# Performance work log

Measured on AMD Instinct MI355X. Metric: run time of the kernel, lower is better.

The kernel has to match this reference:

```python
import jax, jax.numpy as jnp
import numpy as np

B, T, DIM, UNITS, OUT = 64, 240, 512, 1024, 75


def setup_inputs() -> dict:
    key = jax.random.key(0)
    keys = iter(jax.random.split(key, 40))

    def w(shape, scale=0.05):
        return jax.random.normal(next(keys), shape, dtype=jnp.float32) * scale

    inp = {
        "in_audio": w((B, T, DIM), 1.0),   # per-step CNN audio features
        "curr_step": w((B, OUT), 1.0),      # initial motion pose
    }

    def add_cell(name, in_dim, u):
        inp[name + "_Wx"] = w((in_dim, 4 * u))
        inp[name + "_Wh"] = w((u, 4 * u))
        inp[name + "_b"] = jnp.zeros((4 * u,), jnp.float32)

    add_cell("enc1", DIM, UNITS)
    add_cell("enc2", UNITS, UNITS)
    add_cell("enc3", UNITS, UNITS)
    inp["fc_W"] = w((UNITS, DIM))
    inp["fc_b"] = jnp.zeros((DIM,), jnp.float32)
    add_cell("dec1", OUT + DIM, UNITS)
    add_cell("dec2", UNITS, UNITS)
    add_cell("dec3", UNITS, UNITS)
    inp["out_W"] = w((UNITS, OUT))
    inp["out_b"] = jnp.zeros((OUT,), jnp.float32)
    return inp


def _lstm(x, h, c, Wx, Wh, b):
    # standard LSTM cell, gate order i, f, g, o
    z = x @ Wx + h @ Wh + b                      # [B, 4U]
    i, f, g, o = jnp.split(z, 4, axis=-1)
    c_new = jax.nn.sigmoid(f) * c + jax.nn.sigmoid(i) * jnp.tanh(g)
    h_new = jax.nn.sigmoid(o) * jnp.tanh(c_new)
    return h_new, c_new


def reference(in_audio, curr_step,
              enc1_Wx, enc1_Wh, enc1_b,
              enc2_Wx, enc2_Wh, enc2_b,
              enc3_Wx, enc3_Wh, enc3_b,
              fc_W, fc_b,
              dec1_Wx, dec1_Wh, dec1_b,
              dec2_Wx, dec2_Wh, dec2_b,
              dec3_Wx, dec3_Wh, dec3_b,
              out_W, out_b):
    Bn = in_audio.shape[0]
    dt = in_audio.dtype
    zu = jnp.zeros((Bn, UNITS), dt)
    carry = (curr_step,
             zu, zu, zu, zu, zu, zu,   # eh1,ec1,eh2,ec2,eh3,ec3
             zu, zu, zu, zu, zu, zu)   # dh1,dc1,dh2,dc2,dh3,dc3

    def step(carry, x):
        (curr, eh1, ec1, eh2, ec2, eh3, ec3,
         dh1, dc1, dh2, dc2, dh3, dc3) = carry
        eh1, ec1 = _lstm(x, eh1, ec1, enc1_Wx, enc1_Wh, enc1_b)
        eh2, ec2 = _lstm(eh1, eh2, ec2, enc2_Wx, enc2_Wh, enc2_b)
        eh3, ec3 = _lstm(eh2, eh3, ec3, enc3_Wx, enc3_Wh, enc3_b)
        _h = jnp.tanh(eh3 @ fc_W + fc_b)          # bottleneck audio code [B, DIM]
        d_in = jnp.concatenate([curr, _h], axis=-1)  # [B, OUT+DIM]
        dh1, dc1 = _lstm(d_in, dh1, dc1, dec1_Wx, dec1_Wh, dec1_b)
        dh2, dc2 = _lstm(dh1, dh2, dc2, dec2_Wx, dec2_Wh, dec2_b)
        dh3, dc3 = _lstm(dh2, dh3, dc3, dec3_Wx, dec3_Wh, dec3_b)
        y = jax.nn.elu(dh3 @ out_W + out_b)       # next motion step [B, OUT]
        new_carry = (y, eh1, ec1, eh2, ec2, eh3, ec3,
                     dh1, dc1, dh2, dc2, dh3, dc3)
        return new_carry, y

    _, ys = jax.lax.scan(step, carry, jnp.swapaxes(in_audio, 0, 1))
    return jnp.swapaxes(ys, 0, 1)  # [B, T, OUT]
```

## Files before the change

kernel.cpp:

```cpp
#include <hip/hip_runtime.h>
#include <hip/hip_bf16.h>
#include <hip/hip_cooperative_groups.h>

namespace cg = cooperative_groups;

typedef __bf16 bf16;
typedef __bf16 bf16x8 __attribute__((ext_vector_type(8)));
typedef float  floatx4 __attribute__((ext_vector_type(4)));
typedef unsigned int uint32;

#define NB   64
#define NT   240
#define NDIM 512
#define NU   1024
#define NOUT 75
#define NWG  64
#define NTHR 1024

#define HSLOT (64 * 1024)
#define YW    80
#define YSLOT (64 * YW)
#define BW    528
#define BSLOT (64 * BW)

struct Params {
  const float* curr;
  const float* bias[8];
  const bf16*  pk[8];
  const bf16*  audio_bf;
  bf16* hr[6];
  bf16* ybuf;
  bf16* hbot;
  uint32* arrv;
  uint32* gof;
  float* out;
  int rmask;
  int pmask;
};

__device__ __forceinline__ float sigmoidf_(float x) { return 1.f / (1.f + __expf(-x)); }

__device__ __forceinline__ void gbar(uint32* arrv, uint32 sc, int w, int tid)
{
  asm volatile("s_waitcnt vmcnt(0)" ::: "memory");
  __syncthreads();
  if (tid == 0)
    __hip_atomic_store(&arrv[w * 32], sc, __ATOMIC_RELAXED, __HIP_MEMORY_SCOPE_AGENT);
  if (tid < NWG) {
    int spin = 0;
    while (__hip_atomic_load(&arrv[tid * 32], __ATOMIC_RELAXED, __HIP_MEMORY_SCOPE_AGENT) < sc) {
      __builtin_amdgcn_s_sleep(1);
      if (++spin > (1 << 24)) break;
    }
  }
  __syncthreads();
}

template<int ST0, int B1, int ST1, int B2, int ST2, int KTOT, int KREAL>
__device__ void lstm_cell(const bf16* __restrict__ p0, const bf16* __restrict__ p1,
                          const bf16* __restrict__ p2,
                          const bf16* __restrict__ pack, const float* __restrict__ bias,
                          bf16* __restrict__ hout, float& ccr,
                          float (* __restrict__ zbuf)[64][16], bf16 (* __restrict__ hstage)[16],
                          char* __restrict__ cb0, char* __restrict__ cb1,
                          char* __restrict__ cb2, char* __restrict__ cb3,
                          int w, int tid)
{
  const int lane = tid & 63, wid = tid >> 6;
  const int g = wid & 3, v = wid >> 2;
  const int lq = lane >> 4, lr = lane & 15;
  constexpr int NCH = KTOT / 128;

  auto issue = [&](int J, char* bufp) {
    #pragma unroll
    for (int ii = 0; ii < 2; ++ii) {
      const int idx = 2 * wid + ii;
      const int kb  = (idx >> 2) & 3;
      const int sel = idx & 3;
      if (idx < 16) {
        int kq = J * 128 + kb * 32 + lq * 8;
        if constexpr (KREAL < KTOT) { if (kq >= KREAL) kq = B2; }
        const int row = 16 * sel + lr;
        const bf16* src;
        if (kq < B1)      src = p0 + (size_t)row * ST0 + kq;
        else if (kq < B2) src = p1 + (size_t)row * ST1 + (kq - B1);
        else              src = p2 + (size_t)row * ST2 + (kq - B2);
        __builtin_amdgcn_global_load_lds((const uint32*)src,
            (uint32*)(bufp + (kb * 4 + sel) * 1024), 16, 0, 0);
      } else {
        const int kq8 = J * 16 + kb * 4 + lq;
        const bf16* src = pack + ((size_t)kq8 * 4096 + 1024 * sel + 16 * w + lr) * 8;
        __builtin_amdgcn_global_load_lds((const uint32*)src,
            (uint32*)(bufp + 16384 + (kb * 4 + sel) * 1024), 16, 0, 0);
      }
    }
  };

  floatx4 c = {0.f, 0.f, 0.f, 0.f};
  auto compute = [&](const char* bufp) {
    #pragma unroll
    for (int kb = 0; kb < 4; ++kb) {
      bf16x8 af  = *(const bf16x8*)(bufp + (kb * 4 + v) * 1024 + lane * 16);
      bf16x8 bfr = *(const bf16x8*)(bufp + 16384 + (kb * 4 + g) * 1024 + lane * 16);
      c = __builtin_amdgcn_mfma_f32_16x16x32_bf16(af, bfr, c, 0, 0, 0);
    }
  };

  char *pA = cb0, *pB = cb1, *pC = cb2, *pD = cb3;
  issue(0, pA);
  issue(1, pB);
  issue(2, pC);
  for (int J = 0; J + 3 < NCH; ++J) {
    asm volatile("s_waitcnt vmcnt(4)" ::: "memory");
    __builtin_amdgcn_s_barrier();
    asm volatile("" ::: "memory");
    issue(J + 3, pD);
    compute(pA);
    char* t = pA; pA = pB; pB = pC; pC = pD; pD = t;
  }
  asm volatile("s_waitcnt vmcnt(4)" ::: "memory");
  __builtin_amdgcn_s_barrier();
  asm volatile("" ::: "memory");
  compute(pA);
  { char* t = pA; pA = pB; pB = pC; pC = pD; pD = t; }
  asm volatile("s_waitcnt vmcnt(2)" ::: "memory");
  __builtin_amdgcn_s_barrier();
  asm volatile("" ::: "memory");
  compute(pA);
  { char* t = pA; pA = pB; pB = pC; pC = pD; pD = t; }
  asm volatile("s_waitcnt vmcnt(0)" ::: "memory");
  __builtin_amdgcn_s_barrier();
  asm volatile("" ::: "memory");
  compute(pA);

  #pragma unroll
  for (int r = 0; r < 4; ++r)
    zbuf[g][16 * v + lq * 4 + r][lr] = c[r];
  __syncthreads();
  {
    const int m = tid >> 4, u = tid & 15;
    const int uc = 16 * w + u;
    const float zi = zbuf[0][m][u] + bias[uc];
    const float zf = zbuf[1][m][u] + bias[NU + uc];
    const float zg = zbuf[2][m][u] + bias[2 * NU + uc];
    const float zo = zbuf[3][m][u] + bias[3 * NU + uc];
    const float cold = ccr;
    const float cn = sigmoidf_(zf) * cold + sigmoidf_(zi) * tanhf(zg);
    ccr = cn;
    hstage[m][u] = (bf16)(sigmoidf_(zo) * tanhf(cn));
  }
  __syncthreads();
  if (tid < 512) {
    const int m = tid >> 3, up = tid & 7;
    const uint32 vv = *(const uint32*)&hstage[m][2 * up];
    __hip_atomic_store((uint32*)(hout + (size_t)m * NU + 16 * w) + up, vv,
                       __ATOMIC_RELAXED, __HIP_MEMORY_SCOPE_AGENT);
  }
}

template<int NEFF>
__device__ void gemm_small(const bf16* __restrict__ a, const bf16* __restrict__ pack,
                           float (* __restrict__ zbuf)[64][16], int w, int tid)
{
  const int lane = tid & 63, wid = tid >> 6;
  const int v = wid & 3, s = wid >> 2;
  const int lr = lane & 15, lq = lane >> 4;
  const int n0 = 16 * w;

  const bf16* wbase = pack + ((size_t)lq * NEFF + (n0 + lr)) * 8;

  bf16x8 wreg[8];
  #pragma unroll
  for (int i = 0; i < 8; ++i)
    wreg[i] = *(const bf16x8*)(wbase + (size_t)(s + 4 * i) * (4 * NEFF * 8));

  floatx4 c = {0.f,0.f,0.f,0.f};
  const bf16* ab = a + (size_t)(16 * v + lr) * NU;

  bf16x8 xa[2];
  xa[0] = *(const bf16x8*)(ab + s * 32 + lq * 8);
  #pragma unroll
  for (int i = 0; i < 8; ++i) {
    const int cur = i & 1, nxt = cur ^ 1;
    if (i + 1 < 8)
      xa[nxt] = *(const bf16x8*)(ab + (s + 4 * (i + 1)) * 32 + lq * 8);
    c = __builtin_amdgcn_mfma_f32_16x16x32_bf16(xa[cur], wreg[i], c, 0, 0, 0);
  }

  #pragma unroll
  for (int r = 0; r < 4; ++r) zbuf[s][16 * v + lq * 4 + r][lr] = c[r];
  __syncthreads();
}

extern "C" __global__ void __launch_bounds__(NTHR)
dancer_main(Params p)
{
  __shared__ __align__(16) char cbuf[4][32768];
  __shared__ float zbuf[4][64][16];
  __shared__ bf16  hstage[64][16];
  cg::grid_group grid = cg::this_grid();
  const int tid = threadIdx.x;
  const int w = blockIdx.x;
  const int gtid = w * NTHR + tid;
  const int rmask = p.rmask, pmask = p.pmask;

  float cc0 = 0.f, cc1 = 0.f, cc2 = 0.f, cc3 = 0.f, cc4 = 0.f, cc5 = 0.f;

  if (tid == 0) {
    p.arrv[w * 32] = 0;
    if (w == 0) *p.gof = 0;
  }
  for (int i = gtid; i < 6 * NB * NU; i += NWG * NTHR) {
    const int b = i >> 16, off = i & 65535;
    p.hr[b][(size_t)rmask * HSLOT + off] = (bf16)0.f;
  }
  for (int i = gtid; i < NB * YW; i += NWG * NTHR) {
    const int m = i / YW, c = i - m * YW;
    p.ybuf[i] = (c < NOUT) ? (bf16)p.curr[m * NOUT + c] : (bf16)0.f;
  }
  for (int i = gtid; i < (rmask + 1) * NB * 16; i += NWG * NTHR) {
    const int slot = i >> 10, m = (i >> 4) & 63, cix = i & 15;
    p.hbot[(size_t)slot * BSLOT + (size_t)m * BW + 512 + cix] = (bf16)0.f;
  }
  __syncthreads();
  grid.sync();

  uint32 sc = 1;
  for (int t = 0; t < NT; ++t) {
    const int st_ = t & rmask;
    const int sp_ = (t - 1) & rmask;
    __syncthreads();

    lstm_cell<NT * NDIM, NDIM, NU, NDIM, NU, NDIM + NU, NDIM + NU>(
        p.audio_bf + t * NDIM, p.hr[0] + (size_t)sp_ * HSLOT, p.hr[0] + (size_t)sp_ * HSLOT,
        p.pk[0], p.bias[0], p.hr[0] + (size_t)st_ * HSLOT, cc0, zbuf, &hstage[0],
        cbuf[0], cbuf[1], cbuf[2], cbuf[3], w, tid);
    gbar(p.arrv, sc++, w, tid);

    lstm_cell<NU, NU, NU, NU, NU, 2 * NU, 2 * NU>(
        p.hr[0] + (size_t)st_ * HSLOT, p.hr[1] + (size_t)sp_ * HSLOT, p.hr[1] + (size_t)sp_ * HSLOT,
        p.pk[1], p.bias[1], p.hr[1] + (size_t)st_ * HSLOT, cc1, zbuf, &hstage[0],
        cbuf[0], cbuf[1], cbuf[2], cbuf[3], w, tid);
    gbar(p.arrv, sc++, w, tid);

    lstm_cell<NU, NU, NU, NU, NU, 2 * NU, 2 * NU>(
        p.hr[1] + (size_t)st_ * HSLOT, p.hr[2] + (size_t)sp_ * HSLOT, p.hr[2] + (size_t)sp_ * HSLOT,
        p.pk[2], p.bias[2], p.hr[2] + (size_t)st_ * HSLOT, cc2, zbuf, &hstage[0],
        cbuf[0], cbuf[1], cbuf[2], cbuf[3], w, tid);
    gbar(p.arrv, sc++, w, tid);

    if (w < 32) {
      gemm_small<512>(p.hr[2] + (size_t)st_ * HSLOT, p.pk[3], zbuf, w, tid);
      const int m = tid >> 4, u = tid & 15;
      const float z = zbuf[0][m][u] + zbuf[1][m][u] + zbuf[2][m][u] + zbuf[3][m][u]
                      + p.bias[3][16 * w + u];
      hstage[m][u] = (bf16)tanhf(z);
      __syncthreads();
      if (tid < 512) {
        const int m2 = tid >> 3, up = tid & 7;
        const uint32 v = *(const uint32*)&hstage[m2][2 * up];
        __hip_atomic_store((uint32*)(p.hbot + (size_t)st_ * BSLOT + (size_t)m2 * BW + 16 * w) + up,
                           v, __ATOMIC_RELAXED, __HIP_MEMORY_SCOPE_AGENT);
      }
    }
    gbar(p.arrv, sc++, w, tid);

    lstm_cell<YW, YW, BW, YW + BW, NU, 1664, YW + BW + NU>(
        p.ybuf + (size_t)st_ * YSLOT, p.hbot + (size_t)st_ * BSLOT, p.hr[3] + (size_t)sp_ * HSLOT,
        p.pk[4], p.bias[4], p.hr[3] + (size_t)st_ * HSLOT, cc3, zbuf, &hstage[0],
        cbuf[0], cbuf[1], cbuf[2], cbuf[3], w, tid);
    gbar(p.arrv, sc++, w, tid);

    lstm_cell<NU, NU, NU, NU, NU, 2 * NU, 2 * NU>(
        p.hr[3] + (size_t)st_ * HSLOT, p.hr[4] + (size_t)sp_ * HSLOT, p.hr[4] + (size_t)sp_ * HSLOT,
        p.pk[5], p.bias[5], p.hr[4] + (size_t)st_ * HSLOT, cc4, zbuf, &hstage[0],
        cbuf[0], cbuf[1], cbuf[2], cbuf[3], w, tid);
    gbar(p.arrv, sc++, w, tid);

    lstm_cell<NU, NU, NU, NU, NU, 2 * NU, 2 * NU>(
        p.hr[4] + (size_t)st_ * HSLOT, p.hr[5] + (size_t)sp_ * HSLOT, p.hr[5] + (size_t)sp_ * HSLOT,
        p.pk[6], p.bias[6], p.hr[5] + (size_t)st_ * HSLOT, cc5, zbuf, &hstage[0],
        cbuf[0], cbuf[1], cbuf[2], cbuf[3], w, tid);
    gbar(p.arrv, sc++, w, tid);

    if (w < 5) {
      gemm_small<80>(p.hr[5] + (size_t)st_ * HSLOT, p.pk[7], zbuf, w, tid);
      const int m = tid >> 4, u = tid & 15;
      const int n = 16 * w + u;
      float y = 0.f;
      if (n < NOUT) {
        const float z = zbuf[0][m][u] + zbuf[1][m][u] + zbuf[2][m][u] + zbuf[3][m][u]
                        + p.bias[7][n];
        y = (z > 0.f) ? z : (__expf(z) - 1.f);
        p.out[(m * NT + t) * NOUT + n] = y;
      }
      hstage[m][u] = (bf16)y;
      __syncthreads();
      if (tid < 512) {
        const int m2 = tid >> 3, up = tid & 7;
        const uint32 v = *(const uint32*)&hstage[m2][2 * up];
        const size_t sn = (size_t)((t + 1) & rmask) * YSLOT;
        __hip_atomic_store((uint32*)(p.ybuf + sn + (size_t)m2 * YW + 16 * w) + up,
                           v, __ATOMIC_RELAXED, __HIP_MEMORY_SCOPE_AGENT);
      }
    }
    if ((t & pmask) == pmask) grid.sync();
  }
}


__global__ void pack_w(const float* __restrict__ Wx, const float* __restrict__ Wh,
                       int Kx, int KhStart, int Keff, int N, int Neff,
                       bf16* __restrict__ dst)
{
  const int idx = blockIdx.x * blockDim.x + threadIdx.x;
  const int nkb = Keff >> 3;
  const int total = nkb * Neff;
  if (idx >= total) return;
  const int kb = idx / Neff;
  const int n  = idx - kb * Neff;
  bf16x8 o;
  #pragma unroll
  for (int j = 0; j < 8; ++j) {
    const int k = kb * 8 + j;
    float v = 0.f;
    if (n < N) {
      if (k < Kx) v = Wx[(size_t)k * N + n];
      else if (k >= KhStart) v = Wh[(size_t)(k - KhStart) * N + n];
    }
    o[j] = (bf16)v;
  }
  *(bf16x8*)(dst + ((size_t)kb * Neff + n) * 8) = o;
}

__global__ void pack_dec1(const float* __restrict__ Wx, const float* __restrict__ Wh,
                          bf16* __restrict__ dst)
{
  const int idx = blockIdx.x * blockDim.x + threadIdx.x;
  const int total = (1664 >> 3) * 4096;
  if (idx >= total) return;
  const int kb = idx >> 12;
  const int n  = idx & 4095;
  bf16x8 o;
  #pragma unroll
  for (int j = 0; j < 8; ++j) {
    const int k = kb * 8 + j;
    float v = 0.f;
    if (k < 75)                    v = Wx[(size_t)k * 4096 + n];
    else if (k >= 80 && k < 592)   v = Wx[(size_t)(k - 5) * 4096 + n];
    else if (k >= 608 && k < 1632) v = Wh[(size_t)(k - 608) * 4096 + n];
    o[j] = (bf16)v;
  }
  *(bf16x8*)(dst + ((size_t)kb * 4096 + n) * 8) = o;
}

__global__ void cvt_bf16(const float* __restrict__ src, bf16* __restrict__ dst, int n)
{
  const int i = blockIdx.x * blockDim.x + threadIdx.x;
  if (i < n) dst[i] = (bf16)src[i];
}

extern "C" void kernel_launch(void* const* d_in, const int* in_sizes, int n_in,
                              void* d_out, int out_size, void* d_ws, size_t ws_size,
                              hipStream_t stream)
{
  (void)in_sizes; (void)n_in; (void)out_size;

  const float* audio = (const float*)d_in[0];
  const float* curr  = (const float*)d_in[1];
  const float* Wp[8][2] = {
    { (const float*)d_in[2],  (const float*)d_in[3]  },
    { (const float*)d_in[5],  (const float*)d_in[6]  },
    { (const float*)d_in[8],  (const float*)d_in[9]  },
    { (const float*)d_in[11], nullptr                },
    { (const float*)d_in[13], (const float*)d_in[14] },
    { (const float*)d_in[16], (const float*)d_in[17] },
    { (const float*)d_in[19], (const float*)d_in[20] },
    { (const float*)d_in[22], nullptr                },
  };
  const float* bias[8] = {
    (const float*)d_in[4],  (const float*)d_in[7],  (const float*)d_in[10],
    (const float*)d_in[12], (const float*)d_in[15], (const float*)d_in[18],
    (const float*)d_in[21], (const float*)d_in[23],
  };

  const int geo[8][5] = {
    { 512,  512,  1536, 4096, 4096 },
    { 1024, 1024, 2048, 4096, 4096 },
    { 1024, 1024, 2048, 4096, 4096 },
    { 1024, 1024, 1024, 512,  512  },
    { 0,    0,    1664, 4096, 4096 },
    { 1024, 1024, 2048, 4096, 4096 },
    { 1024, 1024, 2048, 4096, 4096 },
    { 1024, 1024, 1024, 75,   80   },
  };

  char* ws = (char*)d_ws;
  size_t off = 0;
  auto take = [&](size_t bytes) -> char* {
    char* p = ws + off;
    off = (off + bytes + 255) & ~(size_t)255;
    return p;
  };

  bf16* audio_bf = (bf16*)take((size_t)NB * NT * NDIM * 2);
  bf16* pk[8];
  for (int i = 0; i < 8; ++i) pk[i] = (bf16*)take((size_t)geo[i][2] * geo[i][4] * 2);
  uint32* arrv = (uint32*)take(64 * 32 * sizeof(uint32));
  uint32* gof  = (uint32*)take(256);

  const size_t slot_bytes = (size_t)6 * HSLOT * 2 + (size_t)YSLOT * 2 + (size_t)BSLOT * 2 + 4096;
  int R = 32;
  while (R > 4 && off + (size_t)R * slot_bytes + (1 << 20) > ws_size) R >>= 1;

  bf16* hr[6];
  for (int i = 0; i < 6; ++i) hr[i] = (bf16*)take((size_t)R * HSLOT * 2);
  bf16* ybuf = (bf16*)take((size_t)R * YSLOT * 2);
  bf16* hbot = (bf16*)take((size_t)R * BSLOT * 2);

  {
    const int n = NB * NT * NDIM;
    cvt_bf16<<<(n + 255) / 256, 256, 0, stream>>>(audio, audio_bf, n);
  }
  for (int i = 0; i < 8; ++i) {
    if (i == 4) {
      const int total = (1664 >> 3) * 4096;
      pack_dec1<<<(total + 255) / 256, 256, 0, stream>>>(Wp[4][0], Wp[4][1], pk[4]);
    } else {
      const int total = (geo[i][2] >> 3) * geo[i][4];
      pack_w<<<(total + 255) / 256, 256, 0, stream>>>(
          Wp[i][0], Wp[i][1], geo[i][0], geo[i][1], geo[i][2], geo[i][3], geo[i][4], pk[i]);
    }
  }

  Params P;
  P.curr = curr;
  for (int i = 0; i < 8; ++i) { P.bias[i] = bias[i]; P.pk[i] = pk[i]; }
  P.audio_bf = audio_bf;
  for (int i = 0; i < 6; ++i) P.hr[i] = hr[i];
  P.ybuf = ybuf;
  P.hbot = hbot;
  P.arrv = arrv;
  P.gof = gof;
  P.out = (float*)d_out;
  P.rmask = R - 1;
  P.pmask = (R >> 1) - 1;

  void* args[] = { &P };
  (void)hipLaunchCooperativeKernel(reinterpret_cast<void*>(dancer_main),
                                   dim3(NWG), dim3(NTHR), args, 0, stream);
}
```

Baseline: 27.36 ms.

## Spread LSTM cells over 256 workgroups with batch-row split and split-K reduction

The persistent cooperative kernel grows from 64 to 256 workgroups. Each workgroup now handles 16 batch rows of one 16-unit slice instead of all 64 rows. Inside a block the 16 waves split the K dimension four ways per gate, load into per-wave LDS ring buffers without block-level barriers, and reduce the partial sums through shared memory before the gate math. The goal is to use more compute units for the serial per-step GEMMs and shorten each step's critical path. In exchange, every weight slice is now read by four workgroups, and each grid barrier has four times as many participants; the spin loop also sleeps longer after a few polls.

```diff
diff --git a/kernel.cpp b/kernel.cpp
--- a/kernel.cpp
+++ b/kernel.cpp
@@ -14,7 +14,7 @@
 #define NDIM 512
 #define NU   1024
 #define NOUT 75
-#define NWG  64
+#define NWG  256
 #define NTHR 1024
 
 #define HSLOT (64 * 1024)
@@ -40,17 +40,18 @@
 
 __device__ __forceinline__ float sigmoidf_(float x) { return 1.f / (1.f + __expf(-x)); }
 
-__device__ __forceinline__ void gbar(uint32* arrv, uint32 sc, int w, int tid)
+__device__ __forceinline__ void gbar(uint32* arrv, uint32 sc, int bid, int tid)
 {
   asm volatile("s_waitcnt vmcnt(0)" ::: "memory");
   __syncthreads();
   if (tid == 0)
-    __hip_atomic_store(&arrv[w * 32], sc, __ATOMIC_RELAXED, __HIP_MEMORY_SCOPE_AGENT);
+    __hip_atomic_store(&arrv[bid * 32], sc, __ATOMIC_RELAXED, __HIP_MEMORY_SCOPE_AGENT);
   if (tid < NWG) {
     int spin = 0;
     while (__hip_atomic_load(&arrv[tid * 32], __ATOMIC_RELAXED, __HIP_MEMORY_SCOPE_AGENT) < sc) {
-      __builtin_amdgcn_s_sleep(1);
-      if (++spin > (1 << 24)) break;
+      if (spin < 4) __builtin_amdgcn_s_sleep(1);
+      else          __builtin_amdgcn_s_sleep(16);
+      if (++spin > (1 << 22)) break;
     }
   }
   __syncthreads();
@@ -62,98 +63,73 @@
                           const bf16* __restrict__ pack, const float* __restrict__ bias,
                           bf16* __restrict__ hout, float& ccr,
                           float (* __restrict__ zbuf)[64][16], bf16 (* __restrict__ hstage)[16],
-                          char* __restrict__ cb0, char* __restrict__ cb1,
-                          char* __restrict__ cb2, char* __restrict__ cb3,
-                          int w, int tid)
+                          char* __restrict__ cbuf,
+                          int w, int R0, int tid)
 {
   const int lane = tid & 63, wid = tid >> 6;
-  const int g = wid & 3, v = wid >> 2;
+  const int g = wid & 3, s = wid >> 2;
   const int lq = lane >> 4, lr = lane & 15;
-  constexpr int NCH = KTOT / 128;
-
-  auto issue = [&](int J, char* bufp) {
-    #pragma unroll
-    for (int ii = 0; ii < 2; ++ii) {
-      const int idx = 2 * wid + ii;
-      const int kb  = (idx >> 2) & 3;
-      const int sel = idx & 3;
-      if (idx < 16) {
-        int kq = J * 128 + kb * 32 + lq * 8;
-        if constexpr (KREAL < KTOT) { if (kq >= KREAL) kq = B2; }
-        const int row = 16 * sel + lr;
-        const bf16* src;
-        if (kq < B1)      src = p0 + (size_t)row * ST0 + kq;
-        else if (kq < B2) src = p1 + (size_t)row * ST1 + (kq - B1);
-        else              src = p2 + (size_t)row * ST2 + (kq - B2);
-        __builtin_amdgcn_global_load_lds((const uint32*)src,
-            (uint32*)(bufp + (kb * 4 + sel) * 1024), 16, 0, 0);
-      } else {
-        const int kq8 = J * 16 + kb * 4 + lq;
-        const bf16* src = pack + ((size_t)kq8 * 4096 + 1024 * sel + 16 * w + lr) * 8;
-        __builtin_amdgcn_global_load_lds((const uint32*)src,
-            (uint32*)(bufp + 16384 + (kb * 4 + sel) * 1024), 16, 0, 0);
-      }
-    }
+  constexpr int NKB = KTOT / 32;
+  constexpr int NITER = NKB / 4;
+
+  char* cb = cbuf + (size_t)wid * 8192;
+
+  const bf16* a0 = p0 + (size_t)(R0 + lr) * ST0;
+  const bf16* a1 = p1 + (size_t)(R0 + lr) * ST1 - B1;
+  const bf16* a2 = p2 + (size_t)(R0 + lr) * ST2 - B2;
+  const bf16* bb = pack + ((size_t)lq * 4096 + 1024 * g + 16 * w + lr) * 8;
+
+  auto issue = [&](int i) {
+    const int kb = 4 * i + s;
+    char* base = cb + (size_t)(i & 3) * 2048;
+    int kq = kb * 32 + lq * 8;
+    if constexpr (KREAL < KTOT) { if (kq >= KREAL) kq = B2; }
+    const bf16* asrc = (kq < B1) ? (a0 + kq) : ((kq < B2) ? (a1 + kq) : (a2 + kq));
+    __builtin_amdgcn_global_load_lds((const uint32*)asrc, (uint32*)base, 16, 0, 0);
+    const bf16* bsrc = bb + (size_t)kb * (4 * 4096 * 8);
+    __builtin_amdgcn_global_load_lds((const uint32*)bsrc, (uint32*)(base + 1024), 16, 0, 0);
   };
 
   floatx4 c = {0.f, 0.f, 0.f, 0.f};
-  auto compute = [&](const char* bufp) {
-    #pragma unroll
-    for (int kb = 0; kb < 4; ++kb) {
-      bf16x8 af  = *(const bf16x8*)(bufp + (kb * 4 + v) * 1024 + lane * 16);
-      bf16x8 bfr = *(const bf16x8*)(bufp + 16384 + (kb * 4 + g) * 1024 + lane * 16);
-      c = __builtin_amdgcn_mfma_f32_16x16x32_bf16(af, bfr, c, 0, 0, 0);
-    }
-  };
-
-  char *pA = cb0, *pB = cb1, *pC = cb2, *pD = cb3;
-  issue(0, pA);
-  issue(1, pB);
-  issue(2, pC);
-  for (int J = 0; J + 3 < NCH; ++J) {
+  auto compute = [&](int i) {
+    const char* base = cb + (size_t)(i & 3) * 2048;
+    bf16x8 af = *(const bf16x8*)(base + lane * 16);
+    bf16x8 bf_ = *(const bf16x8*)(base + 1024 + lane * 16);
+    c = __builtin_amdgcn_mfma_f32_16x16x32_bf16(af, bf_, c, 0, 0, 0);
+  };
+
+  issue(0); issue(1); issue(2);
+  int i = 0;
+  for (; i + 3 < NITER; ++i) {
     asm volatile("s_waitcnt vmcnt(4)" ::: "memory");
-    __builtin_amdgcn_s_barrier();
-    asm volatile("" ::: "memory");
-    issue(J + 3, pD);
-    compute(pA);
-    char* t = pA; pA = pB; pB = pC; pC = pD; pD = t;
-  }
-  asm volatile("s_waitcnt vmcnt(4)" ::: "memory");
-  __builtin_amdgcn_s_barrier();
-  asm volatile("" ::: "memory");
-  compute(pA);
-  { char* t = pA; pA = pB; pB = pC; pC = pD; pD = t; }
-  asm volatile("s_waitcnt vmcnt(2)" ::: "memory");
-  __builtin_amdgcn_s_barrier();
-  asm volatile("" ::: "memory");
-  compute(pA);
-  { char* t = pA; pA = pB; pB = pC; pC = pD; pD = t; }
-  asm volatile("s_waitcnt vmcnt(0)" ::: "memory");
-  __builtin_amdgcn_s_barrier();
-  asm volatile("" ::: "memory");
-  compute(pA);
-
-  #pragma unroll
-  for (int r = 0; r < 4; ++r)
-    zbuf[g][16 * v + lq * 4 + r][lr] = c[r];
-  __syncthreads();
-  {
+    issue(i + 3);
+    compute(i);
+  }
+  asm volatile("s_waitcnt vmcnt(4)" ::: "memory"); compute(i); ++i;
+  asm volatile("s_waitcnt vmcnt(2)" ::: "memory"); compute(i); ++i;
+  asm volatile("s_waitcnt vmcnt(0)" ::: "memory"); compute(i);
+
+  #pragma unroll
+  for (int rr = 0; rr < 4; ++rr)
+    zbuf[s][g * 16 + lq * 4 + rr][lr] = c[rr];
+  __syncthreads();
+  if (tid < 256) {
     const int m = tid >> 4, u = tid & 15;
     const int uc = 16 * w + u;
-    const float zi = zbuf[0][m][u] + bias[uc];
-    const float zf = zbuf[1][m][u] + bias[NU + uc];
-    const float zg = zbuf[2][m][u] + bias[2 * NU + uc];
-    const float zo = zbuf[3][m][u] + bias[3 * NU + uc];
+    const float zi = zbuf[0][m][u]      + zbuf[1][m][u]      + zbuf[2][m][u]      + zbuf[3][m][u]      + bias[uc];
+    const float zf = zbuf[0][16 + m][u] + zbuf[1][16 + m][u] + zbuf[2][16 + m][u] + zbuf[3][16 + m][u] + bias[NU + uc];
+    const float zg = zbuf[0][32 + m][u] + zbuf[1][32 + m][u] + zbuf[2][32 + m][u] + zbuf[3][32 + m][u] + bias[2 * NU + uc];
+    const float zo = zbuf[0][48 + m][u] + zbuf[1][48 + m][u] + zbuf[2][48 + m][u] + zbuf[3][48 + m][u] + bias[3 * NU + uc];
     const float cold = ccr;
     const float cn = sigmoidf_(zf) * cold + sigmoidf_(zi) * tanhf(zg);
     ccr = cn;
     hstage[m][u] = (bf16)(sigmoidf_(zo) * tanhf(cn));
   }
   __syncthreads();
-  if (tid < 512) {
+  if (tid < 128) {
     const int m = tid >> 3, up = tid & 7;
     const uint32 vv = *(const uint32*)&hstage[m][2 * up];
-    __hip_atomic_store((uint32*)(hout + (size_t)m * NU + 16 * w) + up, vv,
+    __hip_atomic_store((uint32*)(hout + (size_t)(R0 + m) * NU + 16 * w) + up, vv,
                        __ATOMIC_RELAXED, __HIP_MEMORY_SCOPE_AGENT);
   }
 }
@@ -195,20 +171,25 @@
 extern "C" __global__ void __launch_bounds__(NTHR)
 dancer_main(Params p)
 {
-  __shared__ __align__(16) char cbuf[4][32768];
+  __shared__ __align__(16) char cbuf[16 * 8192];
   __shared__ float zbuf[4][64][16];
   __shared__ bf16  hstage[64][16];
   cg::grid_group grid = cg::this_grid();
   const int tid = threadIdx.x;
-  const int w = blockIdx.x;
-  const int gtid = w * NTHR + tid;
+  const int bid = blockIdx.x;
+  const int m8 = bid & 7;
+  const int q  = bid >> 3;
+  const int r  = q & 3;
+  const int w  = (q >> 2) * 8 + m8;
+  const int R0 = 16 * r;
+  const int gtid = bid * NTHR + tid;
   const int rmask = p.rmask, pmask = p.pmask;
 
   float cc0 = 0.f, cc1 = 0.f, cc2 = 0.f, cc3 = 0.f, cc4 = 0.f, cc5 = 0.f;
 
   if (tid == 0) {
-    p.arrv[w * 32] = 0;
-    if (w == 0) *p.gof = 0;
+    p.arrv[bid * 32] = 0;
+    if (bid == 0) *p.gof = 0;
   }
   for (int i = gtid; i < 6 * NB * NU; i += NWG * NTHR) {
     const int b = i >> 16, off = i & 65535;
@@ -234,22 +215,22 @@
     lstm_cell<NT * NDIM, NDIM, NU, NDIM, NU, NDIM + NU, NDIM + NU>(
         p.audio_bf + t * NDIM, p.hr[0] + (size_t)sp_ * HSLOT, p.hr[0] + (size_t)sp_ * HSLOT,
         p.pk[0], p.bias[0], p.hr[0] + (size_t)st_ * HSLOT, cc0, zbuf, &hstage[0],
-        cbuf[0], cbuf[1], cbuf[2], cbuf[3], w, tid);
-    gbar(p.arrv, sc++, w, tid);
+        cbuf, w, R0, tid);
+    gbar(p.arrv, sc++, bid, tid);
 
     lstm_cell<NU, NU, NU, NU, NU, 2 * NU, 2 * NU>(
         p.hr[0] + (size_t)st_ * HSLOT, p.hr[1] + (size_t)sp_ * HSLOT, p.hr[1] + (size_t)sp_ * HSLOT,
         p.pk[1], p.bias[1], p.hr[1] + (size_t)st_ * HSLOT, cc1, zbuf, &hstage[0],
-        cbuf[0], cbuf[1], cbuf[2], cbuf[3], w, tid);
-    gbar(p.arrv, sc++, w, tid);
+        cbuf, w, R0, tid);
+    gbar(p.arrv, sc++, bid, tid);
 
     lstm_cell<NU, NU, NU, NU, NU, 2 * NU, 2 * NU>(
         p.hr[1] + (size_t)st_ * HSLOT, p.hr[2] + (size_t)sp_ * HSLOT, p.hr[2] + (size_t)sp_ * HSLOT,
         p.pk[2], p.bias[2], p.hr[2] + (size_t)st_ * HSLOT, cc2, zbuf, &hstage[0],
-        cbuf[0], cbuf[1], cbuf[2], cbuf[3], w, tid);
-    gbar(p.arrv, sc++, w, tid);
-
-    if (w < 32) {
+        cbuf, w, R0, tid);
+    gbar(p.arrv, sc++, bid, tid);
+
+    if (r == 0 && w < 32) {
       gemm_small<512>(p.hr[2] + (size_t)st_ * HSLOT, p.pk[3], zbuf, w, tid);
       const int m = tid >> 4, u = tid & 15;
       const float z = zbuf[0][m][u] + zbuf[1][m][u] + zbuf[2][m][u] + zbuf[3][m][u]
@@ -263,27 +244,27 @@
                            v, __ATOMIC_RELAXED, __HIP_MEMORY_SCOPE_AGENT);
       }
     }
-    gbar(p.arrv, sc++, w, tid);
+    gbar(p.arrv, sc++, bid, tid);
 
     lstm_cell<YW, YW, BW, YW + BW, NU, 1664, YW + BW + NU>(
         p.ybuf + (size_t)st_ * YSLOT, p.hbot + (size_t)st_ * BSLOT, p.hr[3] + (size_t)sp_ * HSLOT,
         p.pk[4], p.bias[4], p.hr[3] + (size_t)st_ * HSLOT, cc3, zbuf, &hstage[0],
-        cbuf[0], cbuf[1], cbuf[2], cbuf[3], w, tid);
-    gbar(p.arrv, sc++, w, tid);
+        cbuf, w, R0, tid);
+    gbar(p.arrv, sc++, bid, tid);
 
     lstm_cell<NU, NU, NU, NU, NU, 2 * NU, 2 * NU>(
         p.hr[3] + (size_t)st_ * HSLOT, p.hr[4] + (size_t)sp_ * HSLOT, p.hr[4] + (size_t)sp_ * HSLOT,
         p.pk[5], p.bias[5], p.hr[4] + (size_t)st_ * HSLOT, cc4, zbuf, &hstage[0],
-        cbuf[0], cbuf[1], cbuf[2], cbuf[3], w, tid);
-    gbar(p.arrv, sc++, w, tid);
+        cbuf, w, R0, tid);
+    gbar(p.arrv, sc++, bid, tid);
 
     lstm_cell<NU, NU, NU, NU, NU, 2 * NU, 2 * NU>(
         p.hr[4] + (size_t)st_ * HSLOT, p.hr[5] + (size_t)sp_ * HSLOT, p.hr[5] + (size_t)sp_ * HSLOT,
         p.pk[6], p.bias[6], p.hr[5] + (size_t)st_ * HSLOT, cc5, zbuf, &hstage[0],
-        cbuf[0], cbuf[1], cbuf[2], cbuf[3], w, tid);
-    gbar(p.arrv, sc++, w, tid);
-
-    if (w < 5) {
+        cbuf, w, R0, tid);
+    gbar(p.arrv, sc++, bid, tid);
+
+    if (r == 0 && w < 5) {
       gemm_small<80>(p.hr[5] + (size_t)st_ * HSLOT, p.pk[7], zbuf, w, tid);
       const int m = tid >> 4, u = tid & 15;
       const int n = 16 * w + u;
@@ -406,7 +387,7 @@
   bf16* audio_bf = (bf16*)take((size_t)NB * NT * NDIM * 2);
   bf16* pk[8];
   for (int i = 0; i < 8; ++i) pk[i] = (bf16*)take((size_t)geo[i][2] * geo[i][4] * 2);
-  uint32* arrv = (uint32*)take(64 * 32 * sizeof(uint32));
+  uint32* arrv = (uint32*)take((size_t)NWG * 32 * sizeof(uint32));
   uint32* gof  = (uint32*)take(256);
 
   const size_t slot_bytes = (size_t)6 * HSLOT * 2 + (size_t)YSLOT * 2 + (size_t)BSLOT * 2 + 4096;
```

Measured after the change: 31.20 ms. +14.0%, slower.
